# Optimization experiments

Measured on AMD Instinct MI355X. Metric: run time of the kernel, lower is better.

The kernel has to match this reference:

```python
import jax, jax.numpy as jnp
import numpy as np

N, C, T, V = 32, 128, 256, 25
K = 5  # temporal kernel size; reflect-pad 2*(K-1)//2 = 4 rows on top
EPS = 1e-5


def _inorm(x):
    # InstanceNorm2d(affine=False): normalize each (n,c) plane over (T,V)
    m = jnp.mean(x, axis=(2, 3), keepdims=True)
    v = jnp.var(x, axis=(2, 3), keepdims=True)
    return (x - m) * jax.lax.rsqrt(v + EPS)


def setup_inputs() -> dict:
    key = jax.random.key(0)
    ks = jax.random.split(key, 5)
    x = jax.random.normal(ks[0], (N, C, T, V), jnp.float32)
    PA = jax.random.normal(ks[1], (V, V), jnp.float32)          # learned adjacency
    Wd = jax.random.normal(ks[2], (C, C), jnp.float32) * 0.05    # 1x1 conv weight (O,I)
    bd = jnp.zeros((C,), jnp.float32)
    Wt = jax.random.normal(ks[3], (C, C, K, 1), jnp.float32) * 0.02  # (O,I,Kt,1)
    bt = jnp.zeros((C,), jnp.float32)
    return {"x": x, "PA": PA, "Wd": Wd, "bd": bd, "Wt": Wt, "bt": bt}


def reference(x, PA, Wd, bd, Wt, bt):
    # GCN unit: x.view(N,C*T,V) @ PA == einsum over last (joint) axis
    g = jnp.einsum('nctv,vw->nctw', x, PA)
    # 1x1 conv (channel GEMM) + bias
    y = jnp.einsum('nctv,oc->notv', g, Wd) + bd[None, :, None, None]
    # instance norm + identity residual (in_c == out_c) + relu
    y = jax.nn.relu(_inorm(y) + x)
    # TCN unit: reflection-pad 4 rows on top of T, conv (5,1) stride 1, instance norm
    yp = jnp.pad(y, ((0, 0), (0, 0), (4, 0), (0, 0)), mode='reflect')
    z = jax.lax.conv_general_dilated(
        yp, Wt, window_strides=(1, 1), padding='VALID',
        dimension_numbers=('NCHW', 'OIHW', 'NCHW')) + bt[None, :, None, None]
    z = _inorm(z)
    # outer residual (identity: in_c == out_c, stride == 1) + relu
    return jax.nn.relu(z + x)
```

## Files before the change

kernel.cpp:

```cpp
#include <hip/hip_runtime.h>


typedef unsigned short u16;
typedef unsigned int   u32;

using short8  = __attribute__((ext_vector_type(8))) short;
using floatx4 = __attribute__((ext_vector_type(4))) float;

#define NBATCH 32
#define CH     128
#define TDIM   256
#define VDIM   25
#define KT     5
#define PLANE  6400
#define EPSF   1e-5f
#define INV_PLANE (1.0f/6400.0f)

__device__ __forceinline__ u16 f2bf(float f) {
    u32 u = __float_as_uint(f);
    return (u16)((u + 0x7fffu + ((u >> 16) & 1u)) >> 16);
}
__device__ __forceinline__ float bf2f(u16 h) {
    return __uint_as_float(((u32)h) << 16);
}
__device__ __forceinline__ void gload_lds16(const void* g, void* l) {
    __builtin_amdgcn_global_load_lds(
        (const __attribute__((address_space(1))) u32*)g,
        (__attribute__((address_space(3))) u32*)l, 16, 0, 0);
}

__global__ __launch_bounds__(256) void k0_init(
    const float* __restrict__ Wd, const float* __restrict__ Wt,
    float* __restrict__ statsY, float* __restrict__ statsZ,
    u16* __restrict__ WdB, u16* __restrict__ Wt_b)
{
    int i = blockIdx.x * 256 + threadIdx.x;
    if (i < 8192) {
        statsY[i] = 0.f;
    } else if (i < 16384) {
        statsZ[i - 8192] = 0.f;
    } else if (i < 32768) {
        int j  = i - 16384;
        int sl = j & 31;
        int o  = (j >> 5) & 127;
        int cc = j >> 12;
        WdB[j] = f2bf(Wd[o * CH + cc * 32 + sl]);
    } else {
        int j  = i - 32768;
        int sl = j & 31;
        int o  = (j >> 5) & 127;
        int r2 = j >> 12;
        int tap = r2 % KT;
        int ic  = r2 / KT;
        int ko = ((o ^ (o >> 2)) & 3);
        int il = (((sl >> 3) ^ ko) << 3) | (sl & 7);
        Wt_b[j] = f2bf(Wt[(o * CH + ic * 32 + il) * KT + tap]);
    }
}

__global__ __launch_bounds__(256) void k1a_gcn(
    const float* __restrict__ x, const float* __restrict__ PA,
    u16* __restrict__ gT)
{
    __shared__ __attribute__((aligned(16))) u32 sG[6800];
    __shared__ __attribute__((aligned(16))) float sPA[700];

    const int tid   = threadIdx.x;
    const int nic   = blockIdx.y;
    const int chunk = blockIdx.x;
    const int c0    = chunk * 400;
    const int cl    = tid >> 3;
    const int tl    = tid & 7;

    for (int i = tid; i < 700; i += 256) {
        int v = i / 28, w = i % 28;
        sPA[i] = (w < VDIM) ? PA[w * VDIM + v] : 0.f;
    }

    const float* xrow = x + (size_t)(nic * 32 + cl) * PLANE + c0 + tl * 50;
    float xr[50];
#pragma unroll
    for (int w = 0; w < 25; ++w) {
        float2 t2 = *(const float2*)(xrow + 2 * w);
        xr[2 * w]     = t2.x;
        xr[2 * w + 1] = t2.y;
    }
    __syncthreads();

    u16* sG16 = (u16*)sG;
#pragma unroll
    for (int v = 0; v < VDIM; ++v) {
        float g0 = 0.f, g1 = 0.f;
        const float* pav = &sPA[v * 28];
#pragma unroll
        for (int w = 0; w < VDIM; ++w) {
            float p = pav[w];
            g0 += xr[w] * p;
            g1 += xr[25 + w] * p;
        }
        int r0 = tl * 50 + v;
        sG16[r0 * 34 + cl]        = f2bf(g0);
        sG16[(r0 + 25) * 34 + cl] = f2bf(g1);
    }
    __syncthreads();

    u32* outd = (u32*)gT;
    const size_t ob = ((size_t)nic * PLANE + c0) * 16;
    for (int j = tid; j < 6400; j += 256) {
        int r = j >> 4, dw = j & 15;
        int q = dw >> 2, b = dw & 3;
        int kr = ((r ^ (r >> 2)) & 3);
        outd[ob + r * 16 + (((q ^ kr) << 2) | b)] = sG[r * 17 + dw];
    }
}

__global__ __launch_bounds__(256) void k1b_mfma(
    const u16* __restrict__ gT, const u16* __restrict__ WdB,
    const float* __restrict__ bd,
    u16* __restrict__ y0b, float* __restrict__ statsY)
{
    __shared__ __attribute__((aligned(16))) char lds[16384];

    const int tid  = threadIdx.x;
    const int wave = tid >> 6;
    const int lane = tid & 63;
    const int l    = lane & 15;
    const int quad = lane >> 4;
    const int n    = blockIdx.y;
    const int c0   = blockIdx.x * 128;
    const int wub  = tid & ~63;

    auto stageB = [&](int cc, char* dst) {
        const char* bsrc = (const char*)gT + ((size_t)(n * 4 + cc) * PLANE + c0) * 64;
#pragma unroll
        for (int it = 0; it < 2; ++it)
            gload_lds16(bsrc + (it * 256 + tid) * 16, dst + (it * 256 + wub) * 16);
    };

    stageB(0, lds);
    __syncthreads();

    floatx4 acc[2][8];
#pragma unroll
    for (int a = 0; a < 2; ++a)
#pragma unroll
        for (int b = 0; b < 8; ++b) acc[a][b] = (floatx4){0.f, 0.f, 0.f, 0.f};

    for (int cc = 0; cc < 4; ++cc) {
        char* const sBc = lds + (cc & 1) * 8192;
        char* const sBn = lds + ((cc + 1) & 1) * 8192;

        const char* abase = (const char*)WdB + cc * 8192 + (wave * 32 + l) * 64 + (quad << 4);
        const short8 a0 = *(const short8*)(abase);
        const short8 a1 = *(const short8*)(abase + 16 * 64);
        __builtin_amdgcn_sched_barrier(0);

        if (cc < 3) stageB(cc + 1, sBn);

#pragma unroll
        for (int ct = 0; ct < 8; ++ct) {
            const int r = ct * 16 + l;
            const short8 b = *(const short8*)(sBc + r * 64 + ((quad ^ ((r ^ (r >> 2)) & 3)) << 4));
            acc[0][ct] = __builtin_amdgcn_mfma_f32_16x16x32_bf16(a0, b, acc[0][ct], 0, 0, 0);
            acc[1][ct] = __builtin_amdgcn_mfma_f32_16x16x32_bf16(a1, b, acc[1][ct], 0, 0, 0);
        }
        __syncthreads();
    }

#pragma unroll
    for (int ot = 0; ot < 2; ++ot) {
#pragma unroll
        for (int reg = 0; reg < 4; ++reg) {
            const int o = wave * 32 + ot * 16 + quad * 4 + reg;
            const float bias = bd[o];
            float s1 = 0.f, s2 = 0.f;
            u16* yp = y0b + (size_t)(n * CH + o) * PLANE + c0 + l;
#pragma unroll
            for (int ct = 0; ct < 8; ++ct) {
                float val = acc[ot][ct][reg] + bias;
                yp[ct * 16] = f2bf(val);
                s1 += val; s2 += val * val;
            }
#pragma unroll
            for (int m = 1; m <= 8; m <<= 1) {
                s1 += __shfl_xor(s1, m, 64);
                s2 += __shfl_xor(s2, m, 64);
            }
            if (l == 0) {
                atomicAdd(&statsY[(n * CH + o) * 2 + 0], s1);
                atomicAdd(&statsY[(n * CH + o) * 2 + 1], s2);
            }
        }
    }
}

__global__ __launch_bounds__(256) void k2_yhat(
    const u16* __restrict__ y0b, const float* __restrict__ x,
    const float* __restrict__ statsY, u16* __restrict__ yhatT)
{
    __shared__ u32 sT[256 * 17];
    __shared__ float sM[32], sR[32];

    const int tid = threadIdx.x;
    const int nic = blockIdx.y;
    const int n   = nic >> 2, ic = nic & 3;
    const int c0  = blockIdx.x * 256;

    if (tid < 32) {
        float a = statsY[(n * CH + ic * 32 + tid) * 2 + 0];
        float b = statsY[(n * CH + ic * 32 + tid) * 2 + 1];
        float m = a * INV_PLANE;
        sM[tid] = m;
        sR[tid] = rsqrtf(b * INV_PLANE - m * m + EPSF);
    }
    __syncthreads();

    u16* sT16 = (u16*)sT;
#pragma unroll
    for (int k = 0; k < 4; ++k) {
        int j  = k * 256 + tid;
        int ch = j >> 5;
        int cb = (j & 31) << 3;
        int g  = (n * CH + ic * 32 + ch) * PLANE + c0 + cb;
        short8 yv = *(const short8*)(y0b + g);
        const float4* xp = (const float4*)(x + g);
        float4 x0 = xp[0], x1 = xp[1];
        float xf[8];
        xf[0] = x0.x; xf[1] = x0.y; xf[2] = x0.z; xf[3] = x0.w;
        xf[4] = x1.x; xf[5] = x1.y; xf[6] = x1.z; xf[7] = x1.w;
        float m = sM[ch], r = sR[ch];
        int wp = ((ch >> 1) ^ ((cb >> 3) & 15));
        u16* dst = sT16 + cb * 34 + wp * 2 + (ch & 1);
#pragma unroll
        for (int e = 0; e < 8; ++e)
            dst[e * 34] = f2bf(fmaxf((bf2f((u16)yv[e]) - m) * r + xf[e], 0.f));
    }
    __syncthreads();

    u32* outd = (u32*)yhatT;
    int obase = (nic * PLANE + c0) * 16;
    for (int idx = tid; idx < 4096; idx += 256) {
        int r = idx >> 4, dw = idx & 15;
        int q = dw >> 2, b = dw & 3;
        u32 val = sT[r * 17 + ((dw ^ (r >> 3)) & 15)];
        int kr = ((r ^ (r >> 2)) & 3);
        outd[obase + r * 16 + (((q ^ kr) << 2) | b)] = val;
    }
}

__global__ __launch_bounds__(256, 3) void k3_mfma(
    const u16* __restrict__ yhatT, const u16* __restrict__ Wt_b,
    const float* __restrict__ bt,
    u16* __restrict__ zb, float* __restrict__ statsZ)
{
    __shared__ __attribute__((aligned(16))) char lds[45056];
    char* const sA = lds;
    char* const sB = lds + 20480;

    const int tid  = threadIdx.x;
    const int wave = tid >> 6;
    const int wr2  = wave >> 1;
    const int wc   = wave & 1;
    const int lane = tid & 63;
    const int l    = lane & 15;
    const int quad = lane >> 4;
    const int id   = blockIdx.x;
    const int xcd  = id & 7;
    const int jj   = id >> 3;
    const int n    = xcd * 4 + jj / 50;
    const int rem  = jj % 50;
    const int oh   = rem / 25;
    const int blk  = rem % 25;
    const int c0   = blk * 256;
    const int wub  = tid & ~63;
    const bool mainp = (blk != 0);

    floatx4 acc[2][8];
#pragma unroll
    for (int a = 0; a < 2; ++a)
#pragma unroll
        for (int b = 0; b < 8; ++b) acc[a][b] = (floatx4){0.f, 0.f, 0.f, 0.f};

    auto bsrcIC = [&](int ic) -> const char* {
        return (const char*)yhatT + ((size_t)(n * 4 + ic) * PLANE) * 64
             + (size_t)(c0 - 100) * 64;
    };

    short8 breg[6];
    if (mainp) {
#pragma unroll
        for (int it = 0; it < 6; ++it)
            breg[it] = *(const short8*)(bsrcIC(0) + (it * 256 + tid) * 16);
    }

    for (int ic = 0; ic < 4; ++ic) {
        __syncthreads();

#pragma unroll
        for (int tap = 0; tap < KT; ++tap)
            gload_lds16((const char*)Wt_b + ic * 40960 + (tap * 128 + oh * 64) * 64 + tid * 16,
                        sA + tap * 4096 + wub * 16);
        __builtin_amdgcn_sched_barrier(0);

        if (mainp) {
#pragma unroll
            for (int it = 0; it < 6; ++it)
                *((short8*)(sB + (it * 256 + tid) * 16)) = breg[it];
            if (ic < 3) {
                const char* nb = bsrcIC(ic + 1);
                __builtin_amdgcn_sched_barrier(0);
#pragma unroll
                for (int it = 0; it < 6; ++it)
                    breg[it] = *(const short8*)(nb + (it * 256 + tid) * 16);
                __builtin_amdgcn_sched_barrier(0);
                asm volatile("s_waitcnt vmcnt(6) lgkmcnt(0)" ::: "memory");
            } else {
                asm volatile("s_waitcnt vmcnt(0) lgkmcnt(0)" ::: "memory");
            }
        } else {
            const char* bsrc = (const char*)yhatT + ((size_t)(n * 4 + ic) * PLANE) * 64;
#pragma unroll
            for (int it = 0; it < 4; ++it)
                gload_lds16(bsrc + (it * 256 + tid) * 16, sB + 6400 + (it * 256 + wub) * 16);
            const u32* bsrcd = (const u32*)bsrc;
            u32* sBd = (u32*)sB;
            for (int idx = tid; idx < 1600; idx += 256) {
                int r = idx >> 4, dw = idx & 15;
                int q = dw >> 2, b = dw & 3;
                int d = 100 - r;
                int tref = (d + 24) / 25;
                int v = r % 25;
                int sc = tref * 25 + v;
                int kd = ((r ^ ((r >> 2) + 3)) & 3);
                int ks = ((sc ^ (sc >> 2)) & 3);
                sBd[r * 16 + (((q ^ kd) << 2) | b)] =
                    bsrcd[sc * 16 + (((q ^ ks) << 2) | b)];
            }
            asm volatile("s_waitcnt vmcnt(0) lgkmcnt(0)" ::: "memory");
        }
        __builtin_amdgcn_s_barrier();
        __builtin_amdgcn_sched_barrier(0);

        __builtin_amdgcn_s_setprio(1);
#pragma unroll
        for (int tap = 0; tap < KT; ++tap) {
            short8 af[2];
#pragma unroll
            for (int ot = 0; ot < 2; ++ot) {
                int ro = wr2 * 32 + ot * 16 + l;
                af[ot] = *(const short8*)(sA + tap * 4096 + ro * 64
                                          + ((quad ^ ((ro ^ (ro >> 2)) & 3)) << 4));
            }
#pragma unroll
            for (int ct = 0; ct < 8; ++ct) {
                int r = wc * 128 + ct * 16 + l + tap * 25;
                const short8 b = *(const short8*)(sB + r * 64
                                          + ((quad ^ ((r ^ ((r >> 2) + 3)) & 3)) << 4));
#pragma unroll
                for (int ot = 0; ot < 2; ++ot)
                    acc[ot][ct] = __builtin_amdgcn_mfma_f32_16x16x32_bf16(af[ot], b, acc[ot][ct], 0, 0, 0);
            }
        }
        __builtin_amdgcn_s_setprio(0);
    }

#pragma unroll
    for (int ot = 0; ot < 2; ++ot) {
#pragma unroll
        for (int reg = 0; reg < 4; ++reg) {
            const int o = oh * 64 + wr2 * 32 + ot * 16 + quad * 4 + reg;
            const float bias = bt[o];
            float s1 = 0.f, s2 = 0.f;
            u16* zp = zb + (size_t)(n * CH + o) * PLANE + c0 + wc * 128 + l;
#pragma unroll
            for (int ct = 0; ct < 8; ++ct) {
                float val = acc[ot][ct][reg] + bias;
                zp[ct * 16] = f2bf(val);
                s1 += val; s2 += val * val;
            }
#pragma unroll
            for (int m = 1; m <= 8; m <<= 1) {
                s1 += __shfl_xor(s1, m, 64);
                s2 += __shfl_xor(s2, m, 64);
            }
            if (l == 0) {
                atomicAdd(&statsZ[(n * CH + o) * 2 + 0], s1);
                atomicAdd(&statsZ[(n * CH + o) * 2 + 1], s2);
            }
        }
    }
}

__global__ __launch_bounds__(256) void k4_final(
    const u16* __restrict__ zb, const float* __restrict__ x,
    const float* __restrict__ statsZ, float* __restrict__ out)
{
    int g = blockIdx.x * 256 + threadIdx.x;
    int p = g / 800;
    float a = statsZ[p * 2 + 0], b = statsZ[p * 2 + 1];
    float m = a * INV_PLANE;
    float r = rsqrtf(b * INV_PLANE - m * m + EPSF);
    short8 zv = *(const short8*)(zb + (size_t)g * 8);
    const float4* xp = (const float4*)x + (size_t)g * 2;
    float4 x0 = xp[0], x1 = xp[1];
    float4 o0, o1;
    o0.x = fmaxf((bf2f((u16)zv[0]) - m) * r + x0.x, 0.f);
    o0.y = fmaxf((bf2f((u16)zv[1]) - m) * r + x0.y, 0.f);
    o0.z = fmaxf((bf2f((u16)zv[2]) - m) * r + x0.z, 0.f);
    o0.w = fmaxf((bf2f((u16)zv[3]) - m) * r + x0.w, 0.f);
    o1.x = fmaxf((bf2f((u16)zv[4]) - m) * r + x1.x, 0.f);
    o1.y = fmaxf((bf2f((u16)zv[5]) - m) * r + x1.y, 0.f);
    o1.z = fmaxf((bf2f((u16)zv[6]) - m) * r + x1.z, 0.f);
    o1.w = fmaxf((bf2f((u16)zv[7]) - m) * r + x1.w, 0.f);
    float4* op = (float4*)out + (size_t)g * 2;
    op[0] = o0;
    op[1] = o1;
}

extern "C" void kernel_launch(void* const* d_in, const int* in_sizes, int n_in,
                              void* d_out, int out_size, void* d_ws, size_t ws_size,
                              hipStream_t stream) {
    const float* x  = (const float*)d_in[0];
    const float* PA = (const float*)d_in[1];
    const float* Wd = (const float*)d_in[2];
    const float* bd = (const float*)d_in[3];
    const float* Wt = (const float*)d_in[4];
    const float* bt = (const float*)d_in[5];
    float* out = (float*)d_out;

    char* wsb = (char*)d_ws;
    u16*   y0b    = (u16*)(wsb);
    u16*   zb     = y0b;
    u16*   gT     = (u16*)(wsb + 52428800);
    u16*   yhatT  = gT;
    float* statsY = (float*)(wsb + 104857600);
    float* statsZ = (float*)(wsb + 104890368);
    u16*   WdB    = (u16*)(wsb + 104923136);
    u16*   Wt_b   = (u16*)(wsb + 104955904);

    k0_init<<<dim3(448), dim3(256), 0, stream>>>(Wd, Wt, statsY, statsZ, WdB, Wt_b);
    k1a_gcn<<<dim3(16, 128), dim3(256), 0, stream>>>(x, PA, gT);
    k1b_mfma<<<dim3(50, 32), dim3(256), 0, stream>>>(gT, WdB, bd, y0b, statsY);
    k2_yhat<<<dim3(25, 128), dim3(256), 0, stream>>>(y0b, x, statsY, yhatT);
    k3_mfma<<<dim3(1600), dim3(256), 0, stream>>>(yhatT, Wt_b, bt, zb, statsZ);
    k4_final<<<dim3(12800), dim3(256), 0, stream>>>(zb, x, statsZ, out);
}
```

Measured before the change: 359.9 us.

## Load conv weights directly from global and double-buffer LDS B tiles

The temporal-conv MFMA kernel stops staging weight (A) fragments through LDS. Each lane now reads its short8 weight fragments straight from global memory, and the swizzle in the weight-prep kernel is removed to match. The B (activation) tile alternates between two LDS buffers across input-channel chunks, which removes the leading __syncthreads and the vmcnt waits. The aim is to cut LDS traffic and barrier stalls, at the cost of global or L2 latency on the A loads inside the MFMA loop. The larger LDS allocation may also reduce occupancy.

```diff
diff --git a/kernel.cpp b/kernel.cpp
--- a/kernel.cpp
+++ b/kernel.cpp
@@ -52,9 +52,7 @@
         int r2 = j >> 12;
         int tap = r2 % KT;
         int ic  = r2 / KT;
-        int ko = ((o ^ (o >> 2)) & 3);
-        int il = (((sl >> 3) ^ ko) << 3) | (sl & 7);
-        Wt_b[j] = f2bf(Wt[(o * CH + ic * 32 + il) * KT + tap]);
+        Wt_b[j] = f2bf(Wt[(o * CH + ic * 32 + sl) * KT + tap]);
     }
 }
 
@@ -253,9 +251,7 @@
     const float* __restrict__ bt,
     u16* __restrict__ zb, float* __restrict__ statsZ)
 {
-    __shared__ __attribute__((aligned(16))) char lds[45056];
-    char* const sA = lds;
-    char* const sB = lds + 20480;
+    __shared__ __attribute__((aligned(16))) char lds[49152];
 
     const int tid  = threadIdx.x;
     const int wave = tid >> 6;
@@ -286,6 +282,9 @@
              + (size_t)(c0 - 100) * 64;
     };
 
+    const char* abase0 = (const char*)Wt_b
+                       + (oh * 64 + wr2 * 32 + l) * 64 + (quad << 4);
+
     short8 breg[6];
     if (mainp) {
 #pragma unroll
@@ -294,36 +293,26 @@
     }
 
     for (int ic = 0; ic < 4; ++ic) {
-        __syncthreads();
-
-#pragma unroll
-        for (int tap = 0; tap < KT; ++tap)
-            gload_lds16((const char*)Wt_b + ic * 40960 + (tap * 128 + oh * 64) * 64 + tid * 16,
-                        sA + tap * 4096 + wub * 16);
-        __builtin_amdgcn_sched_barrier(0);
+        char* const sBc = lds + (ic & 1) * 24576;
 
         if (mainp) {
 #pragma unroll
             for (int it = 0; it < 6; ++it)
-                *((short8*)(sB + (it * 256 + tid) * 16)) = breg[it];
+                *((short8*)(sBc + (it * 256 + tid) * 16)) = breg[it];
             if (ic < 3) {
                 const char* nb = bsrcIC(ic + 1);
-                __builtin_amdgcn_sched_barrier(0);
 #pragma unroll
                 for (int it = 0; it < 6; ++it)
                     breg[it] = *(const short8*)(nb + (it * 256 + tid) * 16);
-                __builtin_amdgcn_sched_barrier(0);
-                asm volatile("s_waitcnt vmcnt(6) lgkmcnt(0)" ::: "memory");
-            } else {
-                asm volatile("s_waitcnt vmcnt(0) lgkmcnt(0)" ::: "memory");
-            }
+            }
+            asm volatile("s_waitcnt lgkmcnt(0)" ::: "memory");
         } else {
             const char* bsrc = (const char*)yhatT + ((size_t)(n * 4 + ic) * PLANE) * 64;
 #pragma unroll
             for (int it = 0; it < 4; ++it)
-                gload_lds16(bsrc + (it * 256 + tid) * 16, sB + 6400 + (it * 256 + wub) * 16);
+                gload_lds16(bsrc + (it * 256 + tid) * 16, sBc + 6400 + (it * 256 + wub) * 16);
             const u32* bsrcd = (const u32*)bsrc;
-            u32* sBd = (u32*)sB;
+            u32* sBd = (u32*)sBc;
             for (int idx = tid; idx < 1600; idx += 256) {
                 int r = idx >> 4, dw = idx & 15;
                 int q = dw >> 2, b = dw & 3;
@@ -346,15 +335,12 @@
         for (int tap = 0; tap < KT; ++tap) {
             short8 af[2];
 #pragma unroll
-            for (int ot = 0; ot < 2; ++ot) {
-                int ro = wr2 * 32 + ot * 16 + l;
-                af[ot] = *(const short8*)(sA + tap * 4096 + ro * 64
-                                          + ((quad ^ ((ro ^ (ro >> 2)) & 3)) << 4));
-            }
+            for (int ot = 0; ot < 2; ++ot)
+                af[ot] = *(const short8*)(abase0 + ic * 40960 + tap * 8192 + ot * 1024);
 #pragma unroll
             for (int ct = 0; ct < 8; ++ct) {
                 int r = wc * 128 + ct * 16 + l + tap * 25;
-                const short8 b = *(const short8*)(sB + r * 64
+                const short8 b = *(const short8*)(sBc + r * 64
                                           + ((quad ^ ((r ^ ((r >> 2) + 3)) & 3)) << 4));
 #pragma unroll
                 for (int ot = 0; ot < 2; ++ot)
```

Result: slower. 408.0 us (+13.4%).
